# Kernel tuning notes

Hardware: AMD Instinct MI355X
Metric: run time of the kernel (lower is better)

The kernel has to match this reference:

```python
import jax, jax.numpy as jnp
import numpy as np

B, T, C, H, HD = 2, 2048, 768, 12, 64  # batch, seq, n_embd, n_head, head_dim
D2 = HD // 2
FF = 4 * C
EPS = 1e-5


def setup_inputs() -> dict:
    key = jax.random.key(0)
    ks = jax.random.split(key, 8)
    s = 0.02  # init scale for weights
    # realistic RoPE cos/sin tables over half the head dim
    pos = jnp.arange(T, dtype=jnp.float32)[:, None]                     # [T,1]
    inv_freq = 1.0 / (10000.0 ** (jnp.arange(D2, dtype=jnp.float32) / D2))
    ang = pos * inv_freq                                                # [T,D2]
    return {
        "x": jax.random.normal(ks[0], (B, T, C), jnp.float32),
        "cos": jnp.cos(ang)[None, :, None, :],                          # [1,T,1,D2]
        "sin": jnp.sin(ang)[None, :, None, :],
        "wq": jax.random.normal(ks[1], (C, C), jnp.float32) * s,        # Linear, bias=False ([in,out])
        "wk": jax.random.normal(ks[2], (C, C), jnp.float32) * s,
        "wv": jax.random.normal(ks[3], (C, C), jnp.float32) * s,
        "wo": jax.random.normal(ks[4], (C, C), jnp.float32) * s,
        "wfc": jax.random.normal(ks[5], (C, FF), jnp.float32) * s,
        "wpr": jax.random.normal(ks[6], (FF, C), jnp.float32) * s,
        "g1": jnp.ones((C,), jnp.float32),
        "g2": jnp.ones((C,), jnp.float32),
    }


def _rmsnorm(x, g):
    return g * (x * jax.lax.rsqrt(jnp.mean(x * x, axis=-1, keepdims=True) + EPS))


def _rope(x, cos, sin):
    # x: [B,T,H,HD]; half-split RoPE as in apply_rotary_emb
    x1, x2 = x[..., :D2], x[..., D2:]
    return jnp.concatenate([x1 * cos + x2 * sin, -x1 * sin + x2 * cos], axis=-1)


def reference(x, cos, sin, wq, wk, wv, wo, wfc, wpr, g1, g2):
    # --- attention sublayer ---
    h = _rmsnorm(x, g1)
    q = (h @ wq).reshape(B, T, H, HD)
    k = (h @ wk).reshape(B, T, H, HD)
    v = (h @ wv).reshape(B, T, H, HD)
    q = _rope(q, cos, sin)
    k = _rope(k, cos, sin)
    scale = 1.0 / np.sqrt(HD).astype(np.float32)
    att = jnp.einsum('bqhd,bkhd->bhqk', q, k) * scale                   # [B,H,T,T]
    causal = jnp.tril(jnp.ones((T, T), dtype=bool))
    att = jnp.where(causal[None, None], att, -jnp.inf)
    p = jax.nn.softmax(att, axis=-1)
    y = jnp.einsum('bhqk,bkhd->bqhd', p, v).reshape(B, T, C)
    x = x + y @ wo
    # --- MLP sublayer: ReLU^2 ---
    h2 = _rmsnorm(x, g2)
    x = x + jnp.square(jax.nn.relu(h2 @ wfc)) @ wpr
    return x
```

## Files before the change

kernel.cpp:

```cpp
#include <hip/hip_runtime.h>
#include <hip/hip_bf16.h>
#include <math.h>

#define Bn 2
#define Tn 2048
#define Cn 768
#define Hn 12
#define HDn 64
#define D2n 32
#define FFn 3072
#define EPSn 1e-5f
#define QKVS (3 * Cn)

typedef short s16x8 __attribute__((ext_vector_type(8)));
typedef float f32x4 __attribute__((ext_vector_type(4)));
typedef unsigned short u16;

__device__ __forceinline__ u16 f2bf(float f) {
    union { float f; unsigned u; } v;
    v.f = f;
    unsigned r = (v.u + 0x7fffu + ((v.u >> 16) & 1u)) >> 16;
    return (u16)r;
}
__device__ __forceinline__ float bf2f(u16 u) {
    union { unsigned u; float f; } v;
    v.u = ((unsigned)u) << 16;
    return v.f;
}
__device__ __forceinline__ unsigned pack2(float a, float b) {
    union { float f; unsigned u; } va, vb;
    va.f = a; vb.f = b;
    return (va.u >> 16) | (vb.u & 0xffff0000u);
}

__device__ __forceinline__ void gl2lds16(const void* g, void* l) {
    __builtin_amdgcn_global_load_lds((const __attribute__((address_space(1))) void*)g,
                                     (__attribute__((address_space(3))) void*)l,
                                     16, 0, 0);
}

__global__ __launch_bounds__(256) void rmsnorm_bf16_kernel(const float* __restrict__ x,
                                                           const float* __restrict__ g,
                                                           u16* __restrict__ out) {
    int row = blockIdx.x;
    const float* xr = x + (size_t)row * Cn;
    u16* orow = out + (size_t)row * Cn;
    int tid = threadIdx.x;
    float v[3];
    float ss = 0.f;
#pragma unroll
    for (int i = 0; i < 3; ++i) {
        v[i] = xr[tid + 256 * i];
        ss += v[i] * v[i];
    }
#pragma unroll
    for (int o = 32; o; o >>= 1) ss += __shfl_xor(ss, o);
    __shared__ float red[4];
    int w = tid >> 6;
    if ((tid & 63) == 0) red[w] = ss;
    __syncthreads();
    float tot = red[0] + red[1] + red[2] + red[3];
    float s = rsqrtf(tot / (float)Cn + EPSn);
#pragma unroll
    for (int i = 0; i < 3; ++i) {
        int c = tid + 256 * i;
        orow[c] = f2bf(g[c] * v[i] * s);
    }
}

__global__ __launch_bounds__(256) void transpose_bf16_kernel(const float* __restrict__ W,
                                                             u16* __restrict__ Wt,
                                                             int K, int N) {
    __shared__ u16 t[32][33];
    int bx = blockIdx.x * 32;
    int by = blockIdx.y * 32;
    int tx = threadIdx.x & 31, ty = threadIdx.x >> 5;
#pragma unroll
    for (int i = 0; i < 4; ++i) {
        int kk = by + ty + i * 8;
        t[ty + i * 8][tx] = f2bf(W[(size_t)kk * N + bx + tx]);
    }
    __syncthreads();
#pragma unroll
    for (int i = 0; i < 4; ++i) {
        int n = bx + ty + i * 8;
        Wt[(size_t)n * K + by + tx] = t[tx][ty + i * 8];
    }
}

template <int EPI, int NI>
__global__ __launch_bounds__(256) void gemm_bt(const u16* __restrict__ A,
                                               const u16* __restrict__ Bt,
                                               const float* __restrict__ R,
                                               void* __restrict__ Cout,
                                               int M, int N, int K) {
    __shared__ u16 As[128 * 32];
    __shared__ u16 Bs[NI * 32 * 32];
    int tid = threadIdx.x;
    int w = tid >> 6, lane = tid & 63;
    int quad = lane >> 4, l16 = lane & 15;
    int bm = blockIdx.y * 128;
    int bn = blockIdx.x * (NI * 32);
    int wrow = (w & 1) * 64, wcol = (w >> 1) * (NI * 16);

    f32x4 acc[4][NI];
#pragma unroll
    for (int i = 0; i < 4; ++i)
#pragma unroll
        for (int j = 0; j < NI; ++j) acc[i][j] = (f32x4){0.f, 0.f, 0.f, 0.f};

    int srow = lane >> 2;
    int scol = (lane & 3) * 8;

    for (int k0 = 0; k0 < K; k0 += 32) {
        __syncthreads();
#pragma unroll
        for (int r = 0; r < 2; ++r) {
            int row = r * 64 + w * 16 + srow;
            gl2lds16(A + (size_t)(bm + row) * K + k0 + scol, &As[(r * 64 + w * 16) * 32]);
        }
#pragma unroll
        for (int r = 0; r < NI / 2; ++r) {
            int row = r * 64 + w * 16 + srow;
            gl2lds16(Bt + (size_t)(bn + row) * K + k0 + scol, &Bs[(r * 64 + w * 16) * 32]);
        }
        __syncthreads();

        s16x8 af[4], bf[NI];
#pragma unroll
        for (int mi = 0; mi < 4; ++mi)
            af[mi] = *(const s16x8*)&As[(wrow + mi * 16 + l16) * 32 + quad * 8];
#pragma unroll
        for (int ni = 0; ni < NI; ++ni)
            bf[ni] = *(const s16x8*)&Bs[(wcol + ni * 16 + l16) * 32 + quad * 8];
#pragma unroll
        for (int mi = 0; mi < 4; ++mi)
#pragma unroll
            for (int ni = 0; ni < NI; ++ni)
                acc[mi][ni] = __builtin_amdgcn_mfma_f32_16x16x32_bf16(af[mi], bf[ni],
                                                                      acc[mi][ni], 0, 0, 0);
    }

#pragma unroll
    for (int mi = 0; mi < 4; ++mi) {
#pragma unroll
        for (int rg = 0; rg < 4; ++rg) {
            size_t row = bm + wrow + mi * 16 + quad * 4 + rg;
#pragma unroll
            for (int ni = 0; ni < NI; ++ni) {
                size_t idx = row * N + bn + wcol + ni * 16 + l16;
                float c = acc[mi][ni][rg];
                if (EPI == 0) {
                    ((float*)Cout)[idx] = c;
                } else if (EPI == 1) {
                    ((float*)Cout)[idx] = c + R[idx];
                } else if (EPI == 2) {
                    c = fmaxf(c, 0.f);
                    ((u16*)Cout)[idx] = f2bf(c * c);
                } else {
                    ((u16*)Cout)[idx] = f2bf(c);
                }
            }
        }
    }
}

__global__ __launch_bounds__(256) void rope_prep_kernel(const u16* __restrict__ qkvb,
                                                        const float* __restrict__ cosp,
                                                        const float* __restrict__ sinp,
                                                        u16* __restrict__ qh,
                                                        u16* __restrict__ kh,
                                                        u16* __restrict__ vtp) {
    __shared__ u16 sT[64][72];
    int tc = blockIdx.x, bh = blockIdx.y;
    int h = bh % Hn, b = bh / Hn;
    int t0 = tc * 64;
    int tid = threadIdx.x;

    int r = tid >> 2;
    int c = (tid & 3) * 8;
    int t = t0 + r;
    size_t srow = (size_t)(b * Tn + t) * QKVS + h * HDn;
    float4 c0 = *(const float4*)&cosp[t * D2n + c];
    float4 c1 = *(const float4*)&cosp[t * D2n + c + 4];
    float4 s0 = *(const float4*)&sinp[t * D2n + c];
    float4 s1 = *(const float4*)&sinp[t * D2n + c + 4];
    float cs[8] = {c0.x, c0.y, c0.z, c0.w, c1.x, c1.y, c1.z, c1.w};
    float sn[8] = {s0.x, s0.y, s0.z, s0.w, s1.x, s1.y, s1.z, s1.w};
#pragma unroll
    for (int tens = 0; tens < 2; ++tens) {
        size_t off = srow + tens * Cn;
        float sc = tens ? 1.f : 0.125f;
        ushort4 lo0 = *(const ushort4*)&qkvb[off + c];
        ushort4 lo1 = *(const ushort4*)&qkvb[off + c + 4];
        ushort4 hi0 = *(const ushort4*)&qkvb[off + c + 32];
        ushort4 hi1 = *(const ushort4*)&qkvb[off + c + 36];
        u16 lo[8] = {lo0.x, lo0.y, lo0.z, lo0.w, lo1.x, lo1.y, lo1.z, lo1.w};
        u16 hi[8] = {hi0.x, hi0.y, hi0.z, hi0.w, hi1.x, hi1.y, hi1.z, hi1.w};
        u16 o1[8], o2[8];
#pragma unroll
        for (int j = 0; j < 8; ++j) {
            float x1 = bf2f(lo[j]), x2 = bf2f(hi[j]);
            o1[j] = f2bf((x1 * cs[j] + x2 * sn[j]) * sc);
            o2[j] = f2bf((-x1 * sn[j] + x2 * cs[j]) * sc);
        }
        u16* dst = (tens ? kh : qh) + ((size_t)bh * Tn + t) * HDn;
        *(ushort4*)&dst[c]      = make_ushort4(o1[0], o1[1], o1[2], o1[3]);
        *(ushort4*)&dst[c + 4]  = make_ushort4(o1[4], o1[5], o1[6], o1[7]);
        *(ushort4*)&dst[c + 32] = make_ushort4(o2[0], o2[1], o2[2], o2[3]);
        *(ushort4*)&dst[c + 36] = make_ushort4(o2[4], o2[5], o2[6], o2[7]);
    }

    int r2 = tid >> 2;
    int cc = (tid & 3) * 16;
    size_t vrow = (size_t)(b * Tn + t0 + r2) * QKVS + h * HDn + 2 * Cn;
#pragma unroll
    for (int j = 0; j < 4; ++j)
        *(ushort4*)&sT[r2][cc + j * 4] = *(const ushort4*)&qkvb[vrow + cc + j * 4];
    __syncthreads();
    int d = tid >> 2;
#pragma unroll
    for (int p = 0; p < 2; ++p) {
        int s = (tid & 3) + p * 4;
        int h2 = s >> 2, qq = s & 3;
        u16 e[8];
#pragma unroll
        for (int j = 0; j < 4; ++j) e[j] = sT[32 * h2 + qq * 4 + j][d];
#pragma unroll
        for (int j = 0; j < 4; ++j) e[4 + j] = sT[32 * h2 + 16 + qq * 4 + j][d];
        size_t outb = ((size_t)bh * HDn + d) * Tn + t0 + s * 8;
        *(ushort4*)&vtp[outb]     = make_ushort4(e[0], e[1], e[2], e[3]);
        *(ushort4*)&vtp[outb + 4] = make_ushort4(e[4], e[5], e[6], e[7]);
    }
}

#define APAD 72

__global__ __launch_bounds__(256) void attn_v3_kernel(const u16* __restrict__ qh,
                                                      const u16* __restrict__ kh,
                                                      const u16* __restrict__ vtp,
                                                      u16* __restrict__ y) {
    __shared__ u16 sQ[64 * APAD];
    __shared__ u16 sK[64 * APAD];
    __shared__ u16 sVp[64 * APAD];

    int qt = 31 - (blockIdx.x / 24);
    int bh = blockIdx.x % 24;
    int h = bh % Hn, b = bh / Hn;
    int qbase = qt * 64;
    int tid = threadIdx.x;
    int lane = tid & 63, w = tid >> 6;
    int quad = lane >> 4, l16 = lane & 15;

    const u16* qg = qh + (size_t)bh * Tn * HDn;
    const u16* kg = kh + (size_t)bh * Tn * HDn;
    const u16* vg = vtp + (size_t)bh * HDn * Tn;

#pragma unroll
    for (int i = 0; i < 2; ++i) {
        int idx = tid + 256 * i;
        int row = idx >> 3, blk = idx & 7;
        *(s16x8*)&sQ[row * APAD + blk * 8] =
            *(const s16x8*)&qg[(size_t)(qbase + row) * HDn + blk * 8];
    }
    __syncthreads();

    s16x8 qf0 = *(const s16x8*)&sQ[(w * 16 + l16) * APAD + quad * 8];
    s16x8 qf1 = *(const s16x8*)&sQ[(w * 16 + l16) * APAD + 32 + quad * 8];

    f32x4 acc[4];
#pragma unroll
    for (int i = 0; i < 4; ++i) acc[i] = (f32x4){0.f, 0.f, 0.f, 0.f};
    float m = -3e38f, l = 0.f;
    const int qloc = w * 16 + l16;

    for (int kbase = 0; kbase <= qbase; kbase += 64) {
        __syncthreads();
#pragma unroll
        for (int i = 0; i < 2; ++i) {
            int idx = tid + 256 * i;
            int row = idx >> 3, blk = idx & 7;
            *(s16x8*)&sK[row * APAD + blk * 8] =
                *(const s16x8*)&kg[(size_t)(kbase + row) * HDn + blk * 8];
            *(s16x8*)&sVp[row * APAD + blk * 8] =
                *(const s16x8*)&vg[(size_t)row * Tn + kbase + blk * 8];
        }
        __syncthreads();

        const bool diag = (kbase == qbase);

        f32x4 st[4];
#pragma unroll
        for (int kb = 0; kb < 4; ++kb) {
            s16x8 kf0 = *(const s16x8*)&sK[(kb * 16 + l16) * APAD + quad * 8];
            s16x8 kf1 = *(const s16x8*)&sK[(kb * 16 + l16) * APAD + 32 + quad * 8];
            f32x4 cfr = (f32x4){0.f, 0.f, 0.f, 0.f};
            cfr = __builtin_amdgcn_mfma_f32_16x16x32_bf16(kf0, qf0, cfr, 0, 0, 0);
            cfr = __builtin_amdgcn_mfma_f32_16x16x32_bf16(kf1, qf1, cfr, 0, 0, 0);
            st[kb] = cfr;
        }

        if (diag) {
#pragma unroll
            for (int kb = 0; kb < 4; ++kb)
#pragma unroll
                for (int rg = 0; rg < 4; ++rg)
                    if (kb * 16 + quad * 4 + rg > qloc) st[kb][rg] = -1e30f;
        }

        float mx = -3e38f;
#pragma unroll
        for (int kb = 0; kb < 4; ++kb)
#pragma unroll
            for (int rg = 0; rg < 4; ++rg) mx = fmaxf(mx, st[kb][rg]);
        mx = fmaxf(mx, __shfl_xor(mx, 16));
        mx = fmaxf(mx, __shfl_xor(mx, 32));
        float mnew = fmaxf(m, mx);
        float alpha = __expf(m - mnew);
        m = mnew;
        float tsum = 0.f;
#pragma unroll
        for (int kb = 0; kb < 4; ++kb) {
#pragma unroll
            for (int rg = 0; rg < 4; ++rg) {
                float p = __expf(st[kb][rg] - mnew);
                st[kb][rg] = p;
                tsum += p;
            }
        }
        tsum += __shfl_xor(tsum, 16);
        tsum += __shfl_xor(tsum, 32);
        l = l * alpha + tsum;

        float aq[4];
#pragma unroll
        for (int rg = 0; rg < 4; ++rg) aq[rg] = __shfl(alpha, quad * 4 + rg);
#pragma unroll
        for (int db = 0; db < 4; ++db)
#pragma unroll
            for (int rg = 0; rg < 4; ++rg) acc[db][rg] *= aq[rg];

        union { s16x8 v; unsigned u[4]; } pa0, pa1;
        pa0.u[0] = pack2(st[0][0], st[0][1]);
        pa0.u[1] = pack2(st[0][2], st[0][3]);
        pa0.u[2] = pack2(st[1][0], st[1][1]);
        pa0.u[3] = pack2(st[1][2], st[1][3]);
        pa1.u[0] = pack2(st[2][0], st[2][1]);
        pa1.u[1] = pack2(st[2][2], st[2][3]);
        pa1.u[2] = pack2(st[3][0], st[3][1]);
        pa1.u[3] = pack2(st[3][2], st[3][3]);

#pragma unroll
        for (int db = 0; db < 4; ++db) {
            int rr = db * 16 + l16;
            s16x8 vf0 = *(const s16x8*)&sVp[rr * APAD + quad * 8];
            s16x8 vf1 = *(const s16x8*)&sVp[rr * APAD + 32 + quad * 8];
            acc[db] = __builtin_amdgcn_mfma_f32_16x16x32_bf16(pa0.v, vf0, acc[db], 0, 0, 0);
            acc[db] = __builtin_amdgcn_mfma_f32_16x16x32_bf16(pa1.v, vf1, acc[db], 0, 0, 0);
        }
    }

    float lq[4];
#pragma unroll
    for (int rg = 0; rg < 4; ++rg) lq[rg] = __shfl(l, quad * 4 + rg);
#pragma unroll
    for (int db = 0; db < 4; ++db) {
#pragma unroll
        for (int rg = 0; rg < 4; ++rg) {
            int row = qbase + w * 16 + quad * 4 + rg;
            y[((size_t)(b * Tn + row) * Hn + h) * HDn + db * 16 + l16] =
                f2bf(acc[db][rg] / lq[rg]);
        }
    }
}

extern "C" void kernel_launch(void* const* d_in, const int* in_sizes, int n_in,
                              void* d_out, int out_size, void* d_ws, size_t ws_size,
                              hipStream_t stream) {
    const float* x    = (const float*)d_in[0];
    const float* cosp = (const float*)d_in[1];
    const float* sinp = (const float*)d_in[2];
    const float* wq   = (const float*)d_in[3];
    const float* wk   = (const float*)d_in[4];
    const float* wv   = (const float*)d_in[5];
    const float* wo   = (const float*)d_in[6];
    const float* wfc  = (const float*)d_in[7];
    const float* wpr  = (const float*)d_in[8];
    const float* g1   = (const float*)d_in[9];
    const float* g2   = (const float*)d_in[10];
    float* out = (float*)d_out;

    const size_t S = (size_t)Bn * Tn * Cn;
    char* W = (char*)d_ws;
    u16* slotA = (u16*)W;
    u16* qkvb  = (u16*)(W + 2 * S);
    u16* yh    = (u16*)(W + 2 * S);
    u16* fbuf  = (u16*)(W + 4 * S);
    u16* qhb   = (u16*)(W + 8 * S);
    u16* khb   = (u16*)(W + 10 * S);
    u16* vtpb  = (u16*)(W + 12 * S);
    float* x1  = (float*)(W + 14 * S);
    u16* wt_qkv = (u16*)(W + 18 * S);
    u16* wt_o   = wt_qkv + (size_t)QKVS * Cn;
    u16* wt_fc  = wt_o + (size_t)Cn * Cn;
    u16* wt_pr  = wt_fc + (size_t)FFn * Cn;

    const int M = Bn * Tn;

    transpose_bf16_kernel<<<dim3(Cn / 32, Cn / 32), 256, 0, stream>>>(wq, wt_qkv, Cn, Cn);
    transpose_bf16_kernel<<<dim3(Cn / 32, Cn / 32), 256, 0, stream>>>(wk, wt_qkv + (size_t)Cn * Cn, Cn, Cn);
    transpose_bf16_kernel<<<dim3(Cn / 32, Cn / 32), 256, 0, stream>>>(wv, wt_qkv + (size_t)2 * Cn * Cn, Cn, Cn);
    transpose_bf16_kernel<<<dim3(Cn / 32, Cn / 32), 256, 0, stream>>>(wo, wt_o, Cn, Cn);
    transpose_bf16_kernel<<<dim3(FFn / 32, Cn / 32), 256, 0, stream>>>(wfc, wt_fc, Cn, FFn);
    transpose_bf16_kernel<<<dim3(Cn / 32, FFn / 32), 256, 0, stream>>>(wpr, wt_pr, FFn, Cn);

    rmsnorm_bf16_kernel<<<M, 256, 0, stream>>>(x, g1, slotA);

    gemm_bt<3, 4><<<dim3(QKVS / 128, M / 128), 256, 0, stream>>>(slotA, wt_qkv, nullptr,
                                                                 qkvb, M, QKVS, Cn);

    rope_prep_kernel<<<dim3(Tn / 64, Bn * Hn), 256, 0, stream>>>(qkvb, cosp, sinp,
                                                                 qhb, khb, vtpb);

    attn_v3_kernel<<<Bn * Hn * (Tn / 64), 256, 0, stream>>>(qhb, khb, vtpb, yh);

    gemm_bt<1, 2><<<dim3(Cn / 64, M / 128), 256, 0, stream>>>(yh, wt_o, x, x1, M, Cn, Cn);

    rmsnorm_bf16_kernel<<<M, 256, 0, stream>>>(x1, g2, slotA);

    gemm_bt<2, 4><<<dim3(FFn / 128, M / 128), 256, 0, stream>>>(slotA, wt_fc, nullptr,
                                                                fbuf, M, FFn, Cn);

    gemm_bt<1, 2><<<dim3(Cn / 64, M / 128), 256, 0, stream>>>(fbuf, wt_pr, x1, out, M, Cn, FFn);
}
```

Before: 305.7 us.

## Split-K the output and down projections with fused residual-reduce and RMSNorm

The attention output projection now runs as a 2-way split-K GEMM that writes fp32 partials. A new kernel sums those partials with the residual and also applies the second RMSNorm. The MLP down projection is split 3-way across two launches, with a final kernel adding the partials and the residual. The aim is more blocks in flight for these narrow (N=768) GEMMs, which launch only 192 blocks each. The cost is extra fp32 partial traffic to memory, additional launches, and the loss of the fused residual epilogue in the old GEMM.

```diff
diff --git a/kernel.cpp b/kernel.cpp
--- a/kernel.cpp
+++ b/kernel.cpp
@@ -66,6 +66,58 @@
         int c = tid + 256 * i;
         orow[c] = f2bf(g[c] * v[i] * s);
     }
+}
+
+__global__ __launch_bounds__(256) void reduce2_rmsnorm_kernel(const float* __restrict__ p0,
+                                                              const float* __restrict__ p1,
+                                                              const float* __restrict__ x,
+                                                              const float* __restrict__ g,
+                                                              float* __restrict__ x1,
+                                                              u16* __restrict__ h2) {
+    int row = blockIdx.x;
+    size_t base = (size_t)row * Cn;
+    int tid = threadIdx.x;
+    float v[3];
+    float ss = 0.f;
+#pragma unroll
+    for (int i = 0; i < 3; ++i) {
+        size_t c = base + tid + 256 * i;
+        float t = x[c] + p0[c] + p1[c];
+        v[i] = t;
+        ss += t * t;
+    }
+#pragma unroll
+    for (int o = 32; o; o >>= 1) ss += __shfl_xor(ss, o);
+    __shared__ float red[4];
+    int w = tid >> 6;
+    if ((tid & 63) == 0) red[w] = ss;
+    __syncthreads();
+    float tot = red[0] + red[1] + red[2] + red[3];
+    float s = rsqrtf(tot / (float)Cn + EPSn);
+#pragma unroll
+    for (int i = 0; i < 3; ++i) {
+        int c = tid + 256 * i;
+        x1[base + c] = v[i];
+        h2[base + c] = f2bf(g[c] * v[i] * s);
+    }
+}
+
+__global__ __launch_bounds__(256) void reduce_final_kernel(const float* __restrict__ q0,
+                                                           const float* __restrict__ qrest,
+                                                           const float* __restrict__ x1,
+                                                           float* __restrict__ out) {
+    const size_t MN = (size_t)Bn * Tn * Cn;
+    size_t i = ((size_t)blockIdx.x * 256 + threadIdx.x) * 4;
+    float4 a = *(const float4*)&x1[i];
+    float4 b = *(const float4*)&q0[i];
+    float4 c = *(const float4*)&qrest[i];
+    float4 d = *(const float4*)&qrest[MN + i];
+    float4 r;
+    r.x = a.x + b.x + c.x + d.x;
+    r.y = a.y + b.y + c.y + d.y;
+    r.z = a.z + b.z + c.z + d.z;
+    r.w = a.w + b.w + c.w + d.w;
+    *(float4*)&out[i] = r;
 }
 
 __global__ __launch_bounds__(256) void transpose_bf16_kernel(const float* __restrict__ W,
@@ -161,6 +213,75 @@
                     ((u16*)Cout)[idx] = f2bf(c);
                 }
             }
+        }
+    }
+}
+
+template <int NI>
+__global__ __launch_bounds__(256) void gemm_bt_part(const u16* __restrict__ A,
+                                                    const u16* __restrict__ Bt,
+                                                    float* __restrict__ P,
+                                                    int M, int N, int lda,
+                                                    int Kc, int kidx0) {
+    __shared__ u16 As[128 * 32];
+    __shared__ u16 Bs[NI * 32 * 32];
+    int tid = threadIdx.x;
+    int w = tid >> 6, lane = tid & 63;
+    int quad = lane >> 4, l16 = lane & 15;
+    int bm = blockIdx.y * 128;
+    int bn = blockIdx.x * (NI * 32);
+    int wrow = (w & 1) * 64, wcol = (w >> 1) * (NI * 16);
+    int kbase = (kidx0 + blockIdx.z) * Kc;
+
+    f32x4 acc[4][NI];
+#pragma unroll
+    for (int i = 0; i < 4; ++i)
+#pragma unroll
+        for (int j = 0; j < NI; ++j) acc[i][j] = (f32x4){0.f, 0.f, 0.f, 0.f};
+
+    int srow = lane >> 2;
+    int scol = (lane & 3) * 8;
+
+    for (int k0 = 0; k0 < Kc; k0 += 32) {
+        __syncthreads();
+#pragma unroll
+        for (int r = 0; r < 2; ++r) {
+            int row = r * 64 + w * 16 + srow;
+            gl2lds16(A + (size_t)(bm + row) * lda + kbase + k0 + scol,
+                     &As[(r * 64 + w * 16) * 32]);
+        }
+#pragma unroll
+        for (int r = 0; r < NI / 2; ++r) {
+            int row = r * 64 + w * 16 + srow;
+            gl2lds16(Bt + (size_t)(bn + row) * lda + kbase + k0 + scol,
+                     &Bs[(r * 64 + w * 16) * 32]);
+        }
+        __syncthreads();
+
+        s16x8 af[4], bf[NI];
+#pragma unroll
+        for (int mi = 0; mi < 4; ++mi)
+            af[mi] = *(const s16x8*)&As[(wrow + mi * 16 + l16) * 32 + quad * 8];
+#pragma unroll
+        for (int ni = 0; ni < NI; ++ni)
+            bf[ni] = *(const s16x8*)&Bs[(wcol + ni * 16 + l16) * 32 + quad * 8];
+#pragma unroll
+        for (int mi = 0; mi < 4; ++mi)
+#pragma unroll
+            for (int ni = 0; ni < NI; ++ni)
+                acc[mi][ni] = __builtin_amdgcn_mfma_f32_16x16x32_bf16(af[mi], bf[ni],
+                                                                      acc[mi][ni], 0, 0, 0);
+    }
+
+    float* Pz = P + (size_t)blockIdx.z * M * N;
+#pragma unroll
+    for (int mi = 0; mi < 4; ++mi) {
+#pragma unroll
+        for (int rg = 0; rg < 4; ++rg) {
+            size_t row = bm + wrow + mi * 16 + quad * 4 + rg;
+#pragma unroll
+            for (int ni = 0; ni < NI; ++ni)
+                Pz[row * N + bn + wcol + ni * 16 + l16] = acc[mi][ni][rg];
         }
     }
 }
@@ -391,10 +512,12 @@
     float* out = (float*)d_out;
 
     const size_t S = (size_t)Bn * Tn * Cn;
+    const size_t MN = S;
     char* W = (char*)d_ws;
     u16* slotA = (u16*)W;
     u16* qkvb  = (u16*)(W + 2 * S);
     u16* yh    = (u16*)(W + 2 * S);
+    float* wop = (float*)(W + 4 * S);
     u16* fbuf  = (u16*)(W + 4 * S);
     u16* qhb   = (u16*)(W + 8 * S);
     u16* khb   = (u16*)(W + 10 * S);
@@ -404,6 +527,9 @@
     u16* wt_o   = wt_qkv + (size_t)QKVS * Cn;
     u16* wt_fc  = wt_o + (size_t)Cn * Cn;
     u16* wt_pr  = wt_fc + (size_t)FFn * Cn;
+    const size_t WB = ((size_t)QKVS * Cn + (size_t)Cn * Cn + 2 * (size_t)FFn * Cn) * 2;
+    float* q0    = (float*)W;
+    float* qrest = (float*)(W + 18 * S + WB);
 
     const int M = Bn * Tn;
 
@@ -424,12 +550,17 @@
 
     attn_v3_kernel<<<Bn * Hn * (Tn / 64), 256, 0, stream>>>(qhb, khb, vtpb, yh);
 
-    gemm_bt<1, 2><<<dim3(Cn / 64, M / 128), 256, 0, stream>>>(yh, wt_o, x, x1, M, Cn, Cn);
-
-    rmsnorm_bf16_kernel<<<M, 256, 0, stream>>>(x1, g2, slotA);
+    gemm_bt_part<2><<<dim3(Cn / 64, M / 128, 2), 256, 0, stream>>>(yh, wt_o, wop,
+                                                                   M, Cn, Cn, Cn / 2, 0);
+    reduce2_rmsnorm_kernel<<<M, 256, 0, stream>>>(wop, wop + MN, x, g2, x1, slotA);
 
     gemm_bt<2, 4><<<dim3(FFn / 128, M / 128), 256, 0, stream>>>(slotA, wt_fc, nullptr,
                                                                 fbuf, M, FFn, Cn);
 
-    gemm_bt<1, 2><<<dim3(Cn / 64, M / 128), 256, 0, stream>>>(fbuf, wt_pr, x1, out, M, Cn, FFn);
-}
+    gemm_bt_part<2><<<dim3(Cn / 64, M / 128, 1), 256, 0, stream>>>(fbuf, wt_pr, q0,
+                                                                   M, Cn, FFn, FFn / 3, 0);
+    gemm_bt_part<2><<<dim3(Cn / 64, M / 128, 2), 256, 0, stream>>>(fbuf, wt_pr, qrest,
+                                                                   M, Cn, FFn, FFn / 3, 1);
+
+    reduce_final_kernel<<<(int)(MN / 1024), 256, 0, stream>>>(q0, qrest, x1, out);
+}
```

Result: no change. 309.2 us (+1.1%).
